# Kernel tuning notes

Hardware: AMD Instinct MI355X
Metric: run time of the kernel (lower is better)

## Reference

```python
import jax, jax.numpy as jnp
import numpy as np
import math

IN_CH = 512
OUT_CH = 512
KSIZE = 3
W_DIM = 512
CONV_SCALE = 1.0 / math.sqrt(IN_CH * KSIZE * KSIZE)
MOD_SCALE = 1.0 / math.sqrt(W_DIM)


def setup_inputs() -> dict:
    key = jax.random.key(0)
    k1, k2, k3, k4 = jax.random.split(key, 4)
    B, H, W = 16, 64, 64
    return {
        "input": jax.random.normal(k1, (B, IN_CH, H, W), dtype=jnp.float32),
        "style": jax.random.normal(k2, (B, W_DIM), dtype=jnp.float32),
        "weight": jax.random.normal(k3, (1, OUT_CH, IN_CH, KSIZE, KSIZE), dtype=jnp.float32),
        "mod_weight": jax.random.normal(k4, (IN_CH, W_DIM), dtype=jnp.float32),
        "mod_bias": jnp.ones((IN_CH,), dtype=jnp.float32),
    }


def reference(input, style, weight, mod_weight, mod_bias):
    B, Cin, H, Wd = input.shape
    # EqualLinear modulation: style -> per-sample, per-input-channel scale
    s = style @ (mod_weight * MOD_SCALE).T + mod_bias  # [B, Cin]
    s = s[:, None, :, None, None]                      # [B,1,Cin,1,1]
    w = CONV_SCALE * weight * s                        # [B,Cout,Cin,k,k]
    demod = jax.lax.rsqrt(jnp.sum(w * w, axis=(2, 3, 4)) + 1e-8)  # [B,Cout]
    w = w * demod[:, :, None, None, None]
    # Grouped conv with groups=batch, same as torch F.conv2d
    w = w.reshape(B * OUT_CH, Cin, KSIZE, KSIZE)
    x = input.reshape(1, B * Cin, H, Wd)
    pad = KSIZE // 2
    out = jax.lax.conv_general_dilated(
        x, w,
        window_strides=(1, 1),
        padding=[(pad, pad), (pad, pad)],
        dimension_numbers=("NCHW", "OIHW", "NCHW"),
        feature_group_count=B,
    )
    return out.reshape(B, OUT_CH, out.shape[2], out.shape[3])
```

## Files before the change

### kernel.cpp

```cpp
#include <hip/hip_runtime.h>
#include <hip/hip_bf16.h>


constexpr float CONV_SCALE = 0.014731391274719738f;
constexpr float MOD_SCALE  = 0.04419417382415922f;

typedef short  bf16x8 __attribute__((ext_vector_type(8)));
typedef float  f32x4  __attribute__((ext_vector_type(4)));

__device__ __forceinline__ unsigned short f2bf(float f) {
  unsigned u = __float_as_uint(f);
  u += 0x7fffu + ((u >> 16) & 1u);
  return (unsigned short)(u >> 16);
}

__device__ __forceinline__ void async16(const void* g, void* l) {
  __builtin_amdgcn_global_load_lds((const __attribute__((address_space(1))) unsigned int*)g,
                                   (__attribute__((address_space(3))) unsigned int*)l,
                                   16, 0, 0);
}

__global__ void k_style(const float* __restrict__ style, const float* __restrict__ mw,
                        const float* __restrict__ mb, float* __restrict__ s) {
  int t = blockIdx.x * 256 + threadIdx.x;
  int b = t & 15, i = t >> 4;
  const float4* st = (const float4*)(style + b * 512);
  const float4* wr = (const float4*)(mw + i * 512);
  float acc = 0.f;
#pragma unroll 8
  for (int j = 0; j < 128; ++j) {
    float4 a = st[j], w4 = wr[j];
    acc += a.x * w4.x + a.y * w4.y + a.z * w4.z + a.w * w4.w;
  }
  s[b * 512 + i] = acc * MOD_SCALE + mb[i];
}

__global__ void k_prepw(const float* __restrict__ w, float* __restrict__ wsq,
                        unsigned short* __restrict__ wt) {
  __shared__ float Wl[2304];
  int t = threadIdx.x;
  size_t base = (size_t)blockIdx.x * 2304;
#pragma unroll
  for (int k = 0; k < 3; ++k) {
    int idx = t + k * 256;
    if (idx < 576) ((float4*)Wl)[idx] = ((const float4*)(w + base))[idx];
  }
  __syncthreads();
  int g = blockIdx.x * 256 + t;
  int ic = g & 511, o = g >> 9;
  float ssq = 0.f;
#pragma unroll
  for (int tap = 0; tap < 9; ++tap) {
    float v = Wl[t * 9 + tap];
    ssq += v * v;
    wt[((size_t)tap * 512 + o) * 512 + ic] = f2bf(v);
  }
  wsq[o * 512 + ic] = ssq;
}

__global__ void k_dscale(const float* __restrict__ s, const float* __restrict__ wsq,
                         float* __restrict__ dscale) {
  int t = blockIdx.x * 256 + threadIdx.x;
  int b = t & 15, o = t >> 4;
  const float4* sq = (const float4*)(wsq + o * 512);
  const float4* sb = (const float4*)(s + b * 512);
  float acc = 0.f;
#pragma unroll 8
  for (int j = 0; j < 128; ++j) {
    float4 q4 = sq[j], s4 = sb[j];
    acc += q4.x * s4.x * s4.x + q4.y * s4.y * s4.y + q4.z * s4.z * s4.z + q4.w * s4.w * s4.w;
  }
  float d = rsqrtf(CONV_SCALE * CONV_SCALE * acc + 1e-8f);
  dscale[b * 512 + o] = d * CONV_SCALE;
}

__global__ void k_xt(const float* __restrict__ x, const float* __restrict__ s,
                     unsigned short* __restrict__ xt) {
  __shared__ float T[64][68];
  int h = blockIdx.x, b = blockIdx.y;
  const float* xp = x + (size_t)b * 512 * 4096 + h * 64;
  unsigned short* xo = xt + ((size_t)(b * 64 + h) * 64) * 512;
  int t = threadIdx.x;
  for (int ic0 = 0; ic0 < 512; ic0 += 64) {
#pragma unroll
    for (int k = 0; k < 4; ++k) {
      int idx = t + k * 256;
      int icl = idx >> 4, c4 = idx & 15;
      int ic = ic0 + icl;
      float4 v = *(const float4*)&xp[(size_t)ic * 4096 + c4 * 4];
      float sc = s[b * 512 + ic];
      v.x *= sc; v.y *= sc; v.z *= sc; v.w *= sc;
      *(float4*)&T[icl][c4 * 4] = v;
    }
    __syncthreads();
#pragma unroll
    for (int c = t; c < 512; c += 256) {
      int wv = c >> 3, ig = (c & 7) * 8;
      unsigned p0 = (unsigned)f2bf(T[ig + 0][wv]) | ((unsigned)f2bf(T[ig + 1][wv]) << 16);
      unsigned p1 = (unsigned)f2bf(T[ig + 2][wv]) | ((unsigned)f2bf(T[ig + 3][wv]) << 16);
      unsigned p2 = (unsigned)f2bf(T[ig + 4][wv]) | ((unsigned)f2bf(T[ig + 5][wv]) << 16);
      unsigned p3 = (unsigned)f2bf(T[ig + 6][wv]) | ((unsigned)f2bf(T[ig + 7][wv]) << 16);
      uint4 pk = {p0, p1, p2, p3};
      *(uint4*)&xo[(size_t)wv * 512 + ic0 + ig] = pk;
    }
    __syncthreads();
  }
}

__global__ __launch_bounds__(256, 2)
void k_conv(const unsigned short* __restrict__ xt, const unsigned short* __restrict__ wt,
            const float* __restrict__ dscale, float* __restrict__ out) {
  __shared__ short Xs[6 * 66 * 32];
  __shared__ short Ws[3 * 128 * 32];

  const int b  = blockIdx.z;
  const int o0 = blockIdx.y * 128;
  const int h0 = blockIdx.x * 4;
  const int t = threadIdx.x;
  const int wave = t >> 6, lane = t & 63;
  const int q = lane >> 4, l16 = lane & 15;

  f32x4 acc[8][4];
#pragma unroll
  for (int i = 0; i < 8; ++i)
#pragma unroll
    for (int j = 0; j < 4; ++j) acc[i][j] = (f32x4){0.f, 0.f, 0.f, 0.f};

  if (t < 192) {
    int r = t >> 5, rem = t & 31;
    int col = (rem >> 4) * 65, ch2 = (rem & 15) * 2;
    *(int*)&Xs[(r * 66 + col) * 32 + ch2] = 0;
  }

  int xrowi[6]; bool xval[6];
#pragma unroll
  for (int j = 0; j < 6; ++j) {
    int c = wave * 6 + j;
    int row = c >> 2;
    int hg = h0 - 1 + row;
    xval[j] = (hg >= 0) && (hg < 64);
    xrowi[j] = c;
    (void)xrowi;
  }

  for (int ic0 = 0; ic0 < 512; ic0 += 32) {
    __syncthreads();
#pragma unroll
    for (int j = 0; j < 6; ++j) {
      int c = wave * 6 + j;
      int row = c >> 2, q16 = c & 3;
      int hg = h0 - 1 + row;
      short* dst = &Xs[(row * 66 + 1 + q16 * 16) * 32];
      if (xval[j]) {
        const unsigned short* src =
            xt + ((size_t)((b * 64 + hg) * 64) + q16 * 16 + (lane >> 2)) * 512 + ic0 + (lane & 3) * 8;
        async16(src, dst);
      } else {
        *(int4*)&dst[lane * 8] = (int4){0, 0, 0, 0};
      }
    }
#pragma unroll
    for (int kh = 0; kh < 3; ++kh) {
      if (kh) __syncthreads();
#pragma unroll
      for (int j = 0; j < 6; ++j) {
        int ci = wave * 6 + j;
        int kw = ci >> 3, oo = ((ci & 7) << 4) + (lane >> 2);
        async16(wt + (((size_t)(kh * 3 + kw) * 512 + o0 + oo) * 512 + ic0 + (lane & 3) * 8),
                &Ws[ci * 512]);
      }
      __syncthreads();
      const short* xbase = &Xs[(wave + kh) * 66 * 32 + q * 8];
#pragma unroll
      for (int kw = 0; kw < 3; ++kw) {
        bf16x8 bfr[4];
#pragma unroll
        for (int ni = 0; ni < 4; ++ni)
          bfr[ni] = *(const bf16x8*)&xbase[(ni * 16 + l16 + kw) * 32];
#pragma unroll
        for (int mi = 0; mi < 8; ++mi) {
          bf16x8 af = *(const bf16x8*)&Ws[(kw * 128 + mi * 16 + l16) * 32 + q * 8];
#pragma unroll
          for (int ni = 0; ni < 4; ++ni)
            acc[mi][ni] = __builtin_amdgcn_mfma_f32_16x16x32_bf16(af, bfr[ni], acc[mi][ni], 0, 0, 0);
        }
      }
    }
  }

  const int h = h0 + wave;
#pragma unroll
  for (int mi = 0; mi < 8; ++mi) {
#pragma unroll
    for (int r = 0; r < 4; ++r) {
      int o_l = mi * 16 + q * 4 + r;
      float ds = dscale[b * 512 + o0 + o_l];
      float* orow = out + ((size_t)(b * 512 + o0 + o_l) * 64 + h) * 64;
#pragma unroll
      for (int ni = 0; ni < 4; ++ni)
        orow[ni * 16 + l16] = acc[mi][ni][r] * ds;
    }
  }
}

extern "C" void kernel_launch(void* const* d_in, const int* in_sizes, int n_in,
                              void* d_out, int out_size, void* d_ws, size_t ws_size,
                              hipStream_t stream) {
  const float* x      = (const float*)d_in[0];
  const float* style  = (const float*)d_in[1];
  const float* weight = (const float*)d_in[2];
  const float* mw     = (const float*)d_in[3];
  const float* mb     = (const float*)d_in[4];
  float* out = (float*)d_out;

  float* s      = (float*)d_ws;
  float* dscale = s + 8192;
  float* wsq    = dscale + 8192;
  unsigned short* wt = (unsigned short*)(wsq + 262144);
  unsigned short* xt = wt + 9 * 512 * 512;

  k_style<<<32, 256, 0, stream>>>(style, mw, mb, s);
  k_prepw<<<1024, 256, 0, stream>>>(weight, wsq, wt);
  k_dscale<<<32, 256, 0, stream>>>(s, wsq, dscale);
  k_xt<<<dim3(64, 16), 256, 0, stream>>>(x, s, xt);
  k_conv<<<dim3(16, 4, 16), 256, 0, stream>>>(xt, wt, dscale, out);
}
```

Baseline: 516.1 us.

## Double-buffer weight tiles and register-prefetch input tile in conv kernel

The conv kernel now double-buffers the weight LDS tile, issuing the next kh/ic slice's async loads before the current MFMA work. The input tile for the next channel block is prefetched into registers and written to LDS after the compute, so both global loads overlap with compute instead of sitting behind barriers. The transpose kernel also switches its LDS padding from 68 to 65 with scalar stores, which should reduce bank conflicts on the column reads. The cost is extra LDS (a second weight buffer) and registers, which could lower occupancy under the 2-block launch bound.

```diff
diff --git a/kernel.cpp b/kernel.cpp
--- a/kernel.cpp
+++ b/kernel.cpp
@@ -76,7 +76,7 @@
 
 __global__ void k_xt(const float* __restrict__ x, const float* __restrict__ s,
                      unsigned short* __restrict__ xt) {
-  __shared__ float T[64][68];
+  __shared__ float T[64][65];
   int h = blockIdx.x, b = blockIdx.y;
   const float* xp = x + (size_t)b * 512 * 4096 + h * 64;
   unsigned short* xo = xt + ((size_t)(b * 64 + h) * 64) * 512;
@@ -85,12 +85,14 @@
 #pragma unroll
     for (int k = 0; k < 4; ++k) {
       int idx = t + k * 256;
-      int icl = idx >> 4, c4 = idx & 15;
+      int icl = idx >> 4, cc = (idx & 15) * 4;
       int ic = ic0 + icl;
-      float4 v = *(const float4*)&xp[(size_t)ic * 4096 + c4 * 4];
+      float4 v = *(const float4*)&xp[(size_t)ic * 4096 + cc];
       float sc = s[b * 512 + ic];
-      v.x *= sc; v.y *= sc; v.z *= sc; v.w *= sc;
-      *(float4*)&T[icl][c4 * 4] = v;
+      T[icl][cc + 0] = v.x * sc;
+      T[icl][cc + 1] = v.y * sc;
+      T[icl][cc + 2] = v.z * sc;
+      T[icl][cc + 3] = v.w * sc;
     }
     __syncthreads();
 #pragma unroll
@@ -111,7 +113,7 @@
 void k_conv(const unsigned short* __restrict__ xt, const unsigned short* __restrict__ wt,
             const float* __restrict__ dscale, float* __restrict__ out) {
   __shared__ short Xs[6 * 66 * 32];
-  __shared__ short Ws[3 * 128 * 32];
+  __shared__ short Ws[2][3 * 128 * 32];
 
   const int b  = blockIdx.z;
   const int o0 = blockIdx.y * 128;
@@ -132,44 +134,56 @@
     *(int*)&Xs[(r * 66 + col) * 32 + ch2] = 0;
   }
 
-  int xrowi[6]; bool xval[6];
+  const int xcol = t >> 2, xq = t & 3;
+  bool rv[6]; size_t xsrc[6]; int xlds[6];
 #pragma unroll
   for (int j = 0; j < 6; ++j) {
-    int c = wave * 6 + j;
-    int row = c >> 2;
-    int hg = h0 - 1 + row;
-    xval[j] = (hg >= 0) && (hg < 64);
-    xrowi[j] = c;
-    (void)xrowi;
-  }
-
-  for (int ic0 = 0; ic0 < 512; ic0 += 32) {
-    __syncthreads();
-#pragma unroll
-    for (int j = 0; j < 6; ++j) {
-      int c = wave * 6 + j;
-      int row = c >> 2, q16 = c & 3;
-      int hg = h0 - 1 + row;
-      short* dst = &Xs[(row * 66 + 1 + q16 * 16) * 32];
-      if (xval[j]) {
-        const unsigned short* src =
-            xt + ((size_t)((b * 64 + hg) * 64) + q16 * 16 + (lane >> 2)) * 512 + ic0 + (lane & 3) * 8;
-        async16(src, dst);
-      } else {
-        *(int4*)&dst[lane * 8] = (int4){0, 0, 0, 0};
-      }
-    }
+    int hg = h0 - 1 + j;
+    rv[j] = (hg >= 0) && (hg < 64);
+    xsrc[j] = ((size_t)((b * 64 + (rv[j] ? hg : 0)) * 64 + xcol)) * 512 + xq * 8;
+    xlds[j] = ((j * 66) + 1 + xcol) * 32 + xq * 8;
+  }
+
+  size_t wsrc[6]; int wlds[6];
+#pragma unroll
+  for (int j = 0; j < 6; ++j) {
+    int ci = wave * 6 + j;
+    int kw = ci >> 3, oo = ((ci & 7) << 4) + (lane >> 2);
+    wsrc[j] = ((size_t)(kw * 512 + o0 + oo)) * 512 + (lane & 3) * 8;
+    wlds[j] = ci * 512;
+  }
+
+  int4 xr[6];
+#pragma unroll
+  for (int j = 0; j < 6; ++j)
+    xr[j] = rv[j] ? *(const int4*)(xt + xsrc[j]) : (int4){0, 0, 0, 0};
+#pragma unroll
+  for (int j = 0; j < 6; ++j)
+    async16(wt + wsrc[j], &Ws[0][wlds[j]]);
+#pragma unroll
+  for (int j = 0; j < 6; ++j)
+    *(int4*)&Xs[xlds[j]] = xr[j];
+  __syncthreads();
+
+  for (int icb = 0; icb < 16; ++icb) {
+    const int ic0 = icb * 32;
 #pragma unroll
     for (int kh = 0; kh < 3; ++kh) {
-      if (kh) __syncthreads();
-#pragma unroll
-      for (int j = 0; j < 6; ++j) {
-        int ci = wave * 6 + j;
-        int kw = ci >> 3, oo = ((ci & 7) << 4) + (lane >> 2);
-        async16(wt + (((size_t)(kh * 3 + kw) * 512 + o0 + oo) * 512 + ic0 + (lane & 3) * 8),
-                &Ws[ci * 512]);
-      }
-      __syncthreads();
+      const bool last = (icb == 15) && (kh == 2);
+      if (!last) {
+        const int nkh = (kh < 2) ? kh + 1 : 0;
+        const int nic = (kh < 2) ? ic0 : ic0 + 32;
+        short* wb = Ws[(icb + kh + 1) & 1];
+#pragma unroll
+        for (int j = 0; j < 6; ++j)
+          async16(wt + wsrc[j] + (size_t)nkh * 786432 + nic, &wb[wlds[j]]);
+      }
+      if (kh == 0 && icb < 15) {
+#pragma unroll
+        for (int j = 0; j < 6; ++j)
+          if (rv[j]) xr[j] = *(const int4*)(xt + xsrc[j] + ic0 + 32);
+      }
+      const short* wsb = Ws[(icb + kh) & 1];
       const short* xbase = &Xs[(wave + kh) * 66 * 32 + q * 8];
 #pragma unroll
       for (int kw = 0; kw < 3; ++kw) {
@@ -179,11 +193,18 @@
           bfr[ni] = *(const bf16x8*)&xbase[(ni * 16 + l16 + kw) * 32];
 #pragma unroll
         for (int mi = 0; mi < 8; ++mi) {
-          bf16x8 af = *(const bf16x8*)&Ws[(kw * 128 + mi * 16 + l16) * 32 + q * 8];
+          bf16x8 af = *(const bf16x8*)&wsb[(kw * 128 + mi * 16 + l16) * 32 + q * 8];
 #pragma unroll
           for (int ni = 0; ni < 4; ++ni)
             acc[mi][ni] = __builtin_amdgcn_mfma_f32_16x16x32_bf16(af, bfr[ni], acc[mi][ni], 0, 0, 0);
         }
+      }
+      __syncthreads();
+      if (kh == 2 && icb < 15) {
+#pragma unroll
+        for (int j = 0; j < 6; ++j)
+          *(int4*)&Xs[xlds[j]] = xr[j];
+        __syncthreads();
       }
     }
   }
```

Result: no change. 525.0 us (+1.7%).
